# Performance work log

Measured on AMD Instinct MI355X. Metric: run time of the kernel, lower is better.

Reference implementation:

```python
import jax, jax.numpy as jnp
import numpy as np

N = 50000      # nodes (square sparse matrix shape[0] == shape[1])
NNZ = 1600000  # edges = N * avg_degree(32)
B = 2          # batch of feature matrices
D = 128        # feature dim


def setup_inputs() -> dict:
    key = jax.random.key(0)
    k1, k2, k3 = jax.random.split(key, 3)
    indices = jax.random.randint(k1, (2, NNZ), 0, N, dtype=jnp.int32)  # [2, nnz] COO (row, col)
    values = jax.random.uniform(k2, (NNZ,), dtype=jnp.float32)          # [nnz] edge values
    b = jax.random.normal(k3, (B, N, D), dtype=jnp.float32)             # [B, N, D] dense features
    return {"indices": indices, "values": values, "n": N, "b": b}


def reference(indices, values, n, b):
    # out = sparse_coo(indices, values, (n, n)) @ b, batched over b's leading dim.
    # True SpMM: gather source-node features, scale by edge value, segment-sum
    # into destination rows. Duplicate indices are summed (same as coalesce()).
    rows, cols = indices[0], indices[1]
    def spmm_one(feat):  # feat: [N, D]
        gathered = values[:, None] * feat[cols]              # [nnz, D]
        return jax.ops.segment_sum(gathered, rows, num_segments=n)  # [N, D]
    return jax.vmap(spmm_one)(b)  # [B, N, D]
```

## Files before the change

kernel.cpp:

```cpp
#include <hip/hip_runtime.h>


#define FEAT_D 128
#define BATCH 2
#define RB_SHIFT 8
#define NB_MAX 256
#define BCAP 10240
#define PART_E 8192
#define PART_T 512

typedef int   iv4 __attribute__((ext_vector_type(4)));
typedef float fv4 __attribute__((ext_vector_type(4)));
typedef unsigned uv2 __attribute__((ext_vector_type(2)));

__device__ inline unsigned short f32_to_bf16_rne(float f) {
  unsigned u = __float_as_uint(f);
  unsigned r = u + 0x7fffu + ((u >> 16) & 1u);
  return (unsigned short)(r >> 16);
}

__global__ void __launch_bounds__(NB_MAX) init_fixed_kernel(
    int* __restrict__ bbase, int* __restrict__ gcur, int nb) {
  const int t = threadIdx.x;
  if (t < nb) {
    bbase[t] = t * BCAP;
    gcur[t] = t * BCAP;
  }
}

__global__ void __launch_bounds__(256) hist_bucket_kernel(
    const int* __restrict__ rows, int nnz, int* __restrict__ bcnt) {
  __shared__ int h[256];
  h[threadIdx.x] = 0;
  __syncthreads();
  const int n4 = nnz >> 2;
  for (int i = blockIdx.x * blockDim.x + threadIdx.x; i < n4;
       i += gridDim.x * blockDim.x) {
    const iv4 r4 = *(reinterpret_cast<const iv4*>(rows) + i);
    atomicAdd(&h[r4.x >> RB_SHIFT], 1);
    atomicAdd(&h[r4.y >> RB_SHIFT], 1);
    atomicAdd(&h[r4.z >> RB_SHIFT], 1);
    atomicAdd(&h[r4.w >> RB_SHIFT], 1);
  }
  if (blockIdx.x == 0 && threadIdx.x < (nnz & 3))
    atomicAdd(&h[rows[(n4 << 2) + threadIdx.x] >> RB_SHIFT], 1);
  __syncthreads();
  if (h[threadIdx.x]) atomicAdd(&bcnt[threadIdx.x], h[threadIdx.x]);
}

__global__ void __launch_bounds__(256) scan_buckets_kernel(
    const int* __restrict__ bcnt, int nb,
    int* __restrict__ bbase, int* __restrict__ gcur) {
  __shared__ int sc[256];
  const int tid = threadIdx.x;
  const int v = (tid < nb) ? bcnt[tid] : 0;
  sc[tid] = v;
  __syncthreads();
  for (int off = 1; off < 256; off <<= 1) {
    int t = (tid >= off) ? sc[tid - off] : 0;
    __syncthreads();
    sc[tid] += t;
    __syncthreads();
  }
  const int excl = sc[tid] - v;
  if (tid < nb) {
    bbase[tid] = excl;
    gcur[tid] = excl;
  }
}

__global__ void __launch_bounds__(PART_T) partition_kernel(
    const int* __restrict__ rows, const int* __restrict__ cols,
    const float* __restrict__ vals, int nnz, int nb,
    int* __restrict__ gcur,
    unsigned long long* __restrict__ cvb) {
  __shared__ int hist[256];
  __shared__ int excl[256];
  __shared__ int cur[256];
  __shared__ int gdst[256];
  __shared__ unsigned long long stage[PART_E];
  __shared__ unsigned char slotb[PART_E];

  const int tid = threadIdx.x;
  const int base = blockIdx.x * PART_E;
  const int cnt = min(PART_E, nnz - base);

  if (tid < 256) hist[tid] = 0;
  __syncthreads();

  for (int k = tid; k < cnt; k += PART_T)
    atomicAdd(&hist[rows[base + k] >> RB_SHIFT], 1);
  __syncthreads();

  if (tid < 256) excl[tid] = hist[tid];
  __syncthreads();
  for (int off = 1; off < 256; off <<= 1) {
    int v = 0;
    if (tid < 256 && tid >= off) v = excl[tid - off];
    __syncthreads();
    if (tid < 256) excl[tid] += v;
    __syncthreads();
  }
  if (tid < 256) {
    const int e = excl[tid] - hist[tid];
    excl[tid] = e;
    cur[tid] = e;
    int gd = 0;
    if (tid < nb && hist[tid] > 0) {
      const int gb = atomicAdd(&gcur[tid], hist[tid]);
      gd = gb - e;
    }
    gdst[tid] = gd;
  }
  __syncthreads();

  for (int k = tid; k < cnt; k += PART_T) {
    const int e = base + k;
    const int r = rows[e];
    const int c = cols[e];
    const float v = __builtin_nontemporal_load(&vals[e]);
    const int b = r >> RB_SHIFT;
    const int pos = atomicAdd(&cur[b], 1);
    stage[pos] = ((unsigned long long)__float_as_uint(v) << 32) |
                 (unsigned)(((r & 255) << 16) | c);
    slotb[pos] = (unsigned char)b;
  }
  __syncthreads();

  for (int i = tid; i < cnt; i += PART_T) {
    const int b = slotb[i];
    cvb[gdst[b] + i] = stage[i];
  }
}

__global__ void __launch_bounds__(256) bucket_sort_kernel(
    const unsigned long long* __restrict__ cvb,
    const int* __restrict__ bbase, const int* __restrict__ gcur,
    int* __restrict__ offsets, int* __restrict__ rowend,
    unsigned long long* __restrict__ cv,
    int n) {
  __shared__ int h[256];
  __shared__ int sc[256];
  __shared__ int cur[256];
  const int tid = threadIdx.x;
  const int b = blockIdx.x;
  const int start = bbase[b];
  const int end = gcur[b];

  h[tid] = 0;
  __syncthreads();
  for (int i = start + tid; i < end; i += 256)
    atomicAdd(&h[((unsigned)cvb[i]) >> 16], 1);
  __syncthreads();
  sc[tid] = h[tid];
  __syncthreads();
  for (int off = 1; off < 256; off <<= 1) {
    int t = (tid >= off) ? sc[tid - off] : 0;
    __syncthreads();
    sc[tid] += t;
    __syncthreads();
  }
  const int excl = sc[tid] - h[tid];
  const int row = (b << RB_SHIFT) + tid;
  if (row < n) {
    offsets[row] = start + excl;
    rowend[row] = start + excl + h[tid];
  }
  cur[tid] = start + excl;
  __syncthreads();
  for (int i = start + tid; i < end; i += 256) {
    const unsigned long long mv = cvb[i];
    const unsigned meta = (unsigned)mv;
    const int pos = atomicAdd(&cur[meta >> 16], 1);
    cv[pos] = (mv & 0xffffffff00000000ull) | (unsigned long long)(meta & 0xffffu);
  }
}

__global__ void __launch_bounds__(256) pack_kernel(
    const float* __restrict__ feat, unsigned short* __restrict__ packed, int n) {
  const int q = blockIdx.x * blockDim.x + threadIdx.x;
  const int total = n * (BATCH * FEAT_D / 4);
  if (q >= total) return;
  const int r = q >> 6;
  const int rem = q & 63;
  const int b = rem >> 5;
  const int d4 = rem & 31;
  const fv4 x = __builtin_nontemporal_load(reinterpret_cast<const fv4*>(
      feat + ((size_t)b * n + r) * FEAT_D + (size_t)d4 * 4));
  unsigned a0 = (unsigned)f32_to_bf16_rne(x.x) | ((unsigned)f32_to_bf16_rne(x.y) << 16);
  unsigned a1 = (unsigned)f32_to_bf16_rne(x.z) | ((unsigned)f32_to_bf16_rne(x.w) << 16);
  uv2 o; o.x = a0; o.y = a1;
  *reinterpret_cast<uv2*>(packed + (size_t)q * 4) = o;
}

__global__ void __launch_bounds__(256) spmm_seg_bf16_kernel(
    const int* __restrict__ offsets, const int* __restrict__ rowend,
    const unsigned long long* __restrict__ cv,
    const unsigned short* __restrict__ packed,
    float* __restrict__ out, int n) {
  const int wid = (int)((blockIdx.x * (unsigned)blockDim.x + threadIdx.x) >> 6);
  if (wid >= n) return;
  const int lane = threadIdx.x & 63;

  int start = __builtin_amdgcn_readfirstlane(offsets[wid]);
  int end = __builtin_amdgcn_readfirstlane(rowend[wid]);

  const unsigned short* pbase = packed + (size_t)lane * 4;

  float4 acc = make_float4(0.f, 0.f, 0.f, 0.f);
#pragma unroll 4
  for (int i = start; i < end; ++i) {
    const unsigned long long p = __builtin_nontemporal_load(&cv[i]);
    const int c = (int)(p & 0xffffu);
    const float v = __uint_as_float((unsigned)(p >> 32));
    const uv2 w = *reinterpret_cast<const uv2*>(pbase + (size_t)c * (BATCH * FEAT_D));
    acc.x += v * __uint_as_float(w.x << 16);
    acc.y += v * __uint_as_float(w.x & 0xffff0000u);
    acc.z += v * __uint_as_float(w.y << 16);
    acc.w += v * __uint_as_float(w.y & 0xffff0000u);
  }
  const int half = lane >> 5;
  const int l32 = lane & 31;
  const size_t bs = (size_t)n * FEAT_D;
  float* dst = out + (size_t)half * bs + (size_t)wid * FEAT_D + (size_t)l32 * 4;
  fv4 o; o.x = acc.x; o.y = acc.y; o.z = acc.z; o.w = acc.w;
  __builtin_nontemporal_store(o, reinterpret_cast<fv4*>(dst));
}

__global__ void __launch_bounds__(256) spmm_atomic_kernel(
    const int* __restrict__ indices, const float* __restrict__ values,
    const float* __restrict__ feat, float* __restrict__ out, int nnz, int n) {
  const long long gid = (long long)blockIdx.x * blockDim.x + threadIdx.x;
  const int lane = (int)(gid & 31);
  const long long e = gid >> 5;
  if (e >= nnz) return;
  const int r = indices[e];
  const int c = indices[(long long)nnz + e];
  const float v = values[e];
  const size_t bs = (size_t)n * FEAT_D;
  for (int b = 0; b < BATCH; ++b) {
    const float4 a = *(reinterpret_cast<const float4*>(feat + b * bs + (size_t)c * FEAT_D) + lane);
    float* dst = out + b * bs + (size_t)r * FEAT_D + (size_t)lane * 4;
    atomicAdd(dst + 0, v * a.x);
    atomicAdd(dst + 1, v * a.y);
    atomicAdd(dst + 2, v * a.z);
    atomicAdd(dst + 3, v * a.w);
  }
}

extern "C" void kernel_launch(void* const* d_in, const int* in_sizes, int n_in,
                              void* d_out, int out_size, void* d_ws, size_t ws_size,
                              hipStream_t stream) {
  const int* indices = (const int*)d_in[0];
  const float* values = (const float*)d_in[1];
  const float* feat = (const float*)d_in[3];
  float* out = (float*)d_out;

  const int nnz = in_sizes[1];
  const int n = out_size / (BATCH * FEAT_D);
  const int nb = (n + 255) >> RB_SHIFT;

  const int* rows = indices;
  const int* cols = indices + nnz;

  size_t off_offsets = 0;
  size_t off_rowend = off_offsets + (size_t)n * 4;
  size_t off_bcnt = off_rowend + (size_t)n * 4;
  size_t off_bbase = off_bcnt + (size_t)NB_MAX * 4;
  size_t off_gcur = off_bbase + (size_t)NB_MAX * 4;
  size_t off_cv = (off_gcur + (size_t)NB_MAX * 4 + 255) & ~(size_t)255;

  const size_t packed_bytes = (size_t)n * BATCH * FEAT_D * 2;
  const size_t cv_fixed = (size_t)nb * BCAP * 8;
  const size_t cv_compact = (size_t)nnz * 8;

  const size_t need_fixed =
      off_cv + cv_fixed + ((cv_fixed > packed_bytes ? cv_fixed : packed_bytes) + 255 & ~(size_t)255);
  const size_t need_compact =
      off_cv + cv_compact + ((cv_compact > packed_bytes ? cv_compact : packed_bytes) + 255 & ~(size_t)255);

  const bool ok_shape = (n <= (NB_MAX << RB_SHIFT)) && (nb <= NB_MAX) &&
                        (nnz / nb + 6000 < BCAP || ws_size >= need_compact);

  if (!ok_shape || ws_size < need_compact) {
    hipMemsetAsync(d_out, 0, (size_t)out_size * sizeof(float), stream);
    const long long total_threads = (long long)nnz * 32;
    const unsigned grid = (unsigned)((total_threads + 255) / 256);
    spmm_atomic_kernel<<<grid, 256, 0, stream>>>(indices, values, feat, out, nnz, n);
    return;
  }

  const bool fixed = (ws_size >= need_fixed) && (nnz / nb + 6000 < BCAP);
  const size_t cv_bytes = fixed ? cv_fixed : cv_compact;
  size_t off_region = (off_cv + cv_bytes + 255) & ~(size_t)255;

  char* ws = (char*)d_ws;
  int* offsets = (int*)(ws + off_offsets);
  int* rowend = (int*)(ws + off_rowend);
  int* bcnt = (int*)(ws + off_bcnt);
  int* bbase = (int*)(ws + off_bbase);
  int* gcur = (int*)(ws + off_gcur);
  unsigned long long* cv = (unsigned long long*)(ws + off_cv);
  unsigned long long* cvb = (unsigned long long*)(ws + off_region);
  unsigned short* packed = (unsigned short*)(ws + off_region);

  if (fixed) {
    init_fixed_kernel<<<1, NB_MAX, 0, stream>>>(bbase, gcur, nb);
  } else {
    hipMemsetAsync(bcnt, 0, (size_t)NB_MAX * 4, stream);
    hist_bucket_kernel<<<512, 256, 0, stream>>>(rows, nnz, bcnt);
    scan_buckets_kernel<<<1, 256, 0, stream>>>(bcnt, nb, bbase, gcur);
  }

  const int part_blocks = (nnz + PART_E - 1) / PART_E;
  partition_kernel<<<part_blocks, PART_T, 0, stream>>>(rows, cols, values, nnz, nb,
                                                       gcur, cvb);
  bucket_sort_kernel<<<nb, 256, 0, stream>>>(cvb, bbase, gcur, offsets, rowend, cv, n);

  const int pack_total = n * (BATCH * FEAT_D / 4);
  pack_kernel<<<(pack_total + 255) / 256, 256, 0, stream>>>(feat, packed, n);

  const unsigned seg_grid = (unsigned)(((long long)n * 64 + 255) / 256);
  spmm_seg_bf16_kernel<<<seg_grid, 256, 0, stream>>>(offsets, rowend, cv, packed, out, n);
}
```

Before: 188.9 us.

## Fuse feature packing into partition kernel and batch SpMM gathers eight-wide

Gives the packed bf16 feature table its own workspace region so it no longer aliases the bucket staging buffer. This lets the pack work run as extra blocks inside the partition launch, saving a kernel launch and overlapping the two bandwidth-bound phases. The SpMM inner loop is manually unrolled by eight: it issues all edge loads, then all gathers, then all FMAs, to raise memory-level parallelism. The cost is more workspace and more register pressure, and the edge-capacity check is loosened.

```diff
diff --git a/kernel.cpp b/kernel.cpp
--- a/kernel.cpp
+++ b/kernel.cpp
@@ -8,6 +8,7 @@
 #define BCAP 10240
 #define PART_E 8192
 #define PART_T 512
+#define PACK_BLOCKS 1024
 
 typedef int   iv4 __attribute__((ext_vector_type(4)));
 typedef float fv4 __attribute__((ext_vector_type(4)));
@@ -17,6 +18,17 @@
   unsigned u = __float_as_uint(f);
   unsigned r = u + 0x7fffu + ((u >> 16) & 1u);
   return (unsigned short)(r >> 16);
+}
+
+__device__ inline uv2 tbl_load(const unsigned short* pbase, unsigned long long p) {
+  return *reinterpret_cast<const uv2*>(pbase + ((size_t)((unsigned)p & 0xffffu) << 8));
+}
+__device__ inline void fma_edge(fv4& acc, unsigned long long p, uv2 w) {
+  const float v = __uint_as_float((unsigned)(p >> 32));
+  acc.x += v * __uint_as_float(w.x << 16);
+  acc.y += v * __uint_as_float(w.x & 0xffff0000u);
+  acc.z += v * __uint_as_float(w.y << 16);
+  acc.w += v * __uint_as_float(w.y & 0xffff0000u);
 }
 
 __global__ void __launch_bounds__(NB_MAX) init_fixed_kernel(
@@ -69,20 +81,14 @@
   }
 }
 
-__global__ void __launch_bounds__(PART_T) partition_kernel(
+__device__ inline void partition_body(
     const int* __restrict__ rows, const int* __restrict__ cols,
     const float* __restrict__ vals, int nnz, int nb,
-    int* __restrict__ gcur,
-    unsigned long long* __restrict__ cvb) {
-  __shared__ int hist[256];
-  __shared__ int excl[256];
-  __shared__ int cur[256];
-  __shared__ int gdst[256];
-  __shared__ unsigned long long stage[PART_E];
-  __shared__ unsigned char slotb[PART_E];
-
+    int* __restrict__ gcur, unsigned long long* __restrict__ cvb,
+    int blk, int* hist, int* excl, int* cur, int* gdst,
+    unsigned long long* stage, unsigned char* slotb) {
   const int tid = threadIdx.x;
-  const int base = blockIdx.x * PART_E;
+  const int base = blk * PART_E;
   const int cnt = min(PART_E, nnz - base);
 
   if (tid < 256) hist[tid] = 0;
@@ -133,12 +139,60 @@
   }
 }
 
+__global__ void __launch_bounds__(PART_T) partition_kernel(
+    const int* __restrict__ rows, const int* __restrict__ cols,
+    const float* __restrict__ vals, int nnz, int nb,
+    int* __restrict__ gcur, unsigned long long* __restrict__ cvb) {
+  __shared__ int hist[256];
+  __shared__ int excl[256];
+  __shared__ int cur[256];
+  __shared__ int gdst[256];
+  __shared__ unsigned long long stage[PART_E];
+  __shared__ unsigned char slotb[PART_E];
+  partition_body(rows, cols, vals, nnz, nb, gcur, cvb, blockIdx.x,
+                 hist, excl, cur, gdst, stage, slotb);
+}
+
+__global__ void __launch_bounds__(PART_T) partpack_kernel(
+    const int* __restrict__ rows, const int* __restrict__ cols,
+    const float* __restrict__ vals, int nnz, int nb,
+    int* __restrict__ gcur, unsigned long long* __restrict__ cvb,
+    const float* __restrict__ feat, unsigned short* __restrict__ packed,
+    int n, int part_blocks) {
+  __shared__ int hist[256];
+  __shared__ int excl[256];
+  __shared__ int cur[256];
+  __shared__ int gdst[256];
+  __shared__ unsigned long long stage[PART_E];
+  __shared__ unsigned char slotb[PART_E];
+
+  if ((int)blockIdx.x < part_blocks) {
+    partition_body(rows, cols, vals, nnz, nb, gcur, cvb, blockIdx.x,
+                   hist, excl, cur, gdst, stage, slotb);
+  } else {
+    const int pb = blockIdx.x - part_blocks;
+    const int npb = gridDim.x - part_blocks;
+    const int total = n * (BATCH * FEAT_D / 4);
+    for (int q = pb * PART_T + threadIdx.x; q < total; q += npb * PART_T) {
+      const int r = q >> 6;
+      const int rem = q & 63;
+      const int b = rem >> 5;
+      const int d4 = rem & 31;
+      const fv4 x = __builtin_nontemporal_load(reinterpret_cast<const fv4*>(
+          feat + ((size_t)b * n + r) * FEAT_D + (size_t)d4 * 4));
+      unsigned a0 = (unsigned)f32_to_bf16_rne(x.x) | ((unsigned)f32_to_bf16_rne(x.y) << 16);
+      unsigned a1 = (unsigned)f32_to_bf16_rne(x.z) | ((unsigned)f32_to_bf16_rne(x.w) << 16);
+      uv2 o; o.x = a0; o.y = a1;
+      *reinterpret_cast<uv2*>(packed + (size_t)q * 4) = o;
+    }
+  }
+}
+
 __global__ void __launch_bounds__(256) bucket_sort_kernel(
     const unsigned long long* __restrict__ cvb,
     const int* __restrict__ bbase, const int* __restrict__ gcur,
     int* __restrict__ offsets, int* __restrict__ rowend,
-    unsigned long long* __restrict__ cv,
-    int n) {
+    unsigned long long* __restrict__ cv, int n) {
   __shared__ int h[256];
   __shared__ int sc[256];
   __shared__ int cur[256];
@@ -207,24 +261,44 @@
 
   const unsigned short* pbase = packed + (size_t)lane * 4;
 
-  float4 acc = make_float4(0.f, 0.f, 0.f, 0.f);
-#pragma unroll 4
-  for (int i = start; i < end; ++i) {
+  fv4 acc; acc.x = 0.f; acc.y = 0.f; acc.z = 0.f; acc.w = 0.f;
+  int i = start;
+  for (; i + 8 <= end; i += 8) {
+    const unsigned long long p0 = __builtin_nontemporal_load(&cv[i + 0]);
+    const unsigned long long p1 = __builtin_nontemporal_load(&cv[i + 1]);
+    const unsigned long long p2 = __builtin_nontemporal_load(&cv[i + 2]);
+    const unsigned long long p3 = __builtin_nontemporal_load(&cv[i + 3]);
+    const unsigned long long p4 = __builtin_nontemporal_load(&cv[i + 4]);
+    const unsigned long long p5 = __builtin_nontemporal_load(&cv[i + 5]);
+    const unsigned long long p6 = __builtin_nontemporal_load(&cv[i + 6]);
+    const unsigned long long p7 = __builtin_nontemporal_load(&cv[i + 7]);
+    const uv2 w0 = tbl_load(pbase, p0);
+    const uv2 w1 = tbl_load(pbase, p1);
+    const uv2 w2 = tbl_load(pbase, p2);
+    const uv2 w3 = tbl_load(pbase, p3);
+    const uv2 w4 = tbl_load(pbase, p4);
+    const uv2 w5 = tbl_load(pbase, p5);
+    const uv2 w6 = tbl_load(pbase, p6);
+    const uv2 w7 = tbl_load(pbase, p7);
+    fma_edge(acc, p0, w0);
+    fma_edge(acc, p1, w1);
+    fma_edge(acc, p2, w2);
+    fma_edge(acc, p3, w3);
+    fma_edge(acc, p4, w4);
+    fma_edge(acc, p5, w5);
+    fma_edge(acc, p6, w6);
+    fma_edge(acc, p7, w7);
+  }
+  for (; i < end; ++i) {
     const unsigned long long p = __builtin_nontemporal_load(&cv[i]);
-    const int c = (int)(p & 0xffffu);
-    const float v = __uint_as_float((unsigned)(p >> 32));
-    const uv2 w = *reinterpret_cast<const uv2*>(pbase + (size_t)c * (BATCH * FEAT_D));
-    acc.x += v * __uint_as_float(w.x << 16);
-    acc.y += v * __uint_as_float(w.x & 0xffff0000u);
-    acc.z += v * __uint_as_float(w.y << 16);
-    acc.w += v * __uint_as_float(w.y & 0xffff0000u);
-  }
+    fma_edge(acc, p, tbl_load(pbase, p));
+  }
+
   const int half = lane >> 5;
   const int l32 = lane & 31;
   const size_t bs = (size_t)n * FEAT_D;
   float* dst = out + (size_t)half * bs + (size_t)wid * FEAT_D + (size_t)l32 * 4;
-  fv4 o; o.x = acc.x; o.y = acc.y; o.z = acc.z; o.w = acc.w;
-  __builtin_nontemporal_store(o, reinterpret_cast<fv4*>(dst));
+  __builtin_nontemporal_store(acc, reinterpret_cast<fv4*>(dst));
 }
 
 __global__ void __launch_bounds__(256) spmm_atomic_kernel(
@@ -248,6 +322,8 @@
   }
 }
 
+static inline size_t align256(size_t x) { return (x + 255) & ~(size_t)255; }
+
 extern "C" void kernel_launch(void* const* d_in, const int* in_sizes, int n_in,
                               void* d_out, int out_size, void* d_ws, size_t ws_size,
                               hipStream_t stream) {
@@ -268,31 +344,31 @@
   size_t off_bcnt = off_rowend + (size_t)n * 4;
   size_t off_bbase = off_bcnt + (size_t)NB_MAX * 4;
   size_t off_gcur = off_bbase + (size_t)NB_MAX * 4;
-  size_t off_cv = (off_gcur + (size_t)NB_MAX * 4 + 255) & ~(size_t)255;
+  size_t off_cv = align256(off_gcur + (size_t)NB_MAX * 4);
 
   const size_t packed_bytes = (size_t)n * BATCH * FEAT_D * 2;
   const size_t cv_fixed = (size_t)nb * BCAP * 8;
   const size_t cv_compact = (size_t)nnz * 8;
 
-  const size_t need_fixed =
-      off_cv + cv_fixed + ((cv_fixed > packed_bytes ? cv_fixed : packed_bytes) + 255 & ~(size_t)255);
-  const size_t need_compact =
-      off_cv + cv_compact + ((cv_compact > packed_bytes ? cv_compact : packed_bytes) + 255 & ~(size_t)255);
-
-  const bool ok_shape = (n <= (NB_MAX << RB_SHIFT)) && (nb <= NB_MAX) &&
-                        (nnz / nb + 6000 < BCAP || ws_size >= need_compact);
-
-  if (!ok_shape || ws_size < need_compact) {
+  const size_t offA_cvb = align256(off_cv + cv_fixed);
+  const size_t offA_packed = align256(offA_cvb + cv_fixed);
+  const size_t needA = offA_packed + packed_bytes;
+  const size_t offB_region = align256(off_cv + cv_fixed);
+  const size_t needB = offB_region + (cv_fixed > packed_bytes ? cv_fixed : packed_bytes);
+  const size_t offC_region = align256(off_cv + cv_compact);
+  const size_t needC = offC_region + (cv_compact > packed_bytes ? cv_compact : packed_bytes);
+
+  const int avg = nnz / (nb > 0 ? nb : 1);
+  const bool cap_ok = (avg + avg / 8 + 256) < BCAP;
+  const bool shape_ok = (n <= (NB_MAX << RB_SHIFT)) && (nb <= NB_MAX) && (n <= 65536);
+
+  if (!shape_ok || ws_size < needC) {
     hipMemsetAsync(d_out, 0, (size_t)out_size * sizeof(float), stream);
     const long long total_threads = (long long)nnz * 32;
     const unsigned grid = (unsigned)((total_threads + 255) / 256);
     spmm_atomic_kernel<<<grid, 256, 0, stream>>>(indices, values, feat, out, nnz, n);
     return;
   }
-
-  const bool fixed = (ws_size >= need_fixed) && (nnz / nb + 6000 < BCAP);
-  const size_t cv_bytes = fixed ? cv_fixed : cv_compact;
-  size_t off_region = (off_cv + cv_bytes + 255) & ~(size_t)255;
 
   char* ws = (char*)d_ws;
   int* offsets = (int*)(ws + off_offsets);
@@ -301,25 +377,38 @@
   int* bbase = (int*)(ws + off_bbase);
   int* gcur = (int*)(ws + off_gcur);
   unsigned long long* cv = (unsigned long long*)(ws + off_cv);
-  unsigned long long* cvb = (unsigned long long*)(ws + off_region);
-  unsigned short* packed = (unsigned short*)(ws + off_region);
-
-  if (fixed) {
+
+  const int part_blocks = (nnz + PART_E - 1) / PART_E;
+  const int pack_total = n * (BATCH * FEAT_D / 4);
+
+  if (cap_ok && ws_size >= needA) {
+    unsigned long long* cvb = (unsigned long long*)(ws + offA_cvb);
+    unsigned short* packed = (unsigned short*)(ws + offA_packed);
     init_fixed_kernel<<<1, NB_MAX, 0, stream>>>(bbase, gcur, nb);
+    partpack_kernel<<<part_blocks + PACK_BLOCKS, PART_T, 0, stream>>>(
+        rows, cols, values, nnz, nb, gcur, cvb, feat, packed, n, part_blocks);
+    bucket_sort_kernel<<<nb, 256, 0, stream>>>(cvb, bbase, gcur, offsets, rowend, cv, n);
+    const unsigned seg_grid = (unsigned)(((long long)n * 64 + 255) / 256);
+    spmm_seg_bf16_kernel<<<seg_grid, 256, 0, stream>>>(offsets, rowend, cv, packed, out, n);
+  } else if (cap_ok && ws_size >= needB) {
+    unsigned long long* cvb = (unsigned long long*)(ws + offB_region);
+    unsigned short* packed = (unsigned short*)(ws + offB_region);
+    init_fixed_kernel<<<1, NB_MAX, 0, stream>>>(bbase, gcur, nb);
+    partition_kernel<<<part_blocks, PART_T, 0, stream>>>(rows, cols, values, nnz, nb, gcur, cvb);
+    bucket_sort_kernel<<<nb, 256, 0, stream>>>(cvb, bbase, gcur, offsets, rowend, cv, n);
+    pack_kernel<<<(pack_total + 255) / 256, 256, 0, stream>>>(feat, packed, n);
+    const unsigned seg_grid = (unsigned)(((long long)n * 64 + 255) / 256);
+    spmm_seg_bf16_kernel<<<seg_grid, 256, 0, stream>>>(offsets, rowend, cv, packed, out, n);
   } else {
+    unsigned long long* cvb = (unsigned long long*)(ws + offC_region);
+    unsigned short* packed = (unsigned short*)(ws + offC_region);
     hipMemsetAsync(bcnt, 0, (size_t)NB_MAX * 4, stream);
     hist_bucket_kernel<<<512, 256, 0, stream>>>(rows, nnz, bcnt);
     scan_buckets_kernel<<<1, 256, 0, stream>>>(bcnt, nb, bbase, gcur);
-  }
-
-  const int part_blocks = (nnz + PART_E - 1) / PART_E;
-  partition_kernel<<<part_blocks, PART_T, 0, stream>>>(rows, cols, values, nnz, nb,
-                                                       gcur, cvb);
-  bucket_sort_kernel<<<nb, 256, 0, stream>>>(cvb, bbase, gcur, offsets, rowend, cv, n);
-
-  const int pack_total = n * (BATCH * FEAT_D / 4);
-  pack_kernel<<<(pack_total + 255) / 256, 256, 0, stream>>>(feat, packed, n);
-
-  const unsigned seg_grid = (unsigned)(((long long)n * 64 + 255) / 256);
-  spmm_seg_bf16_kernel<<<seg_grid, 256, 0, stream>>>(offsets, rowend, cv, packed, out, n);
-}
+    partition_kernel<<<part_blocks, PART_T, 0, stream>>>(rows, cols, values, nnz, nb, gcur, cvb);
+    bucket_sort_kernel<<<nb, 256, 0, stream>>>(cvb, bbase, gcur, offsets, rowend, cv, n);
+    pack_kernel<<<(pack_total + 255) / 256, 256, 0, stream>>>(feat, packed, n);
+    const unsigned seg_grid = (unsigned)(((long long)n * 64 + 255) / 256);
+    spmm_seg_bf16_kernel<<<seg_grid, 256, 0, stream>>>(offsets, rowend, cv, packed, out, n);
+  }
+}
```

Result: faster. 164.7 us (-12.8%).
